# Kernel tuning notes

Hardware: AMD Instinct MI355X
Metric: run time of the kernel (lower is better)

The kernel has to match this reference:

```python
import jax, jax.numpy as jnp
import numpy as np

N_NODES = 100000
N_EDGES = 1600000  # undirected edges (incidence rows)
F_IN, HID, N_CLS = 500, 256, 40
K_ITERS = 5
LAMBDA1 = 3.0
LAMBDA2 = 3.0


def setup_inputs() -> dict:
    key = jax.random.key(0)
    k1, k2, k3, k4, k5 = jax.random.split(key, 5)
    x = jax.random.normal(k1, (N_NODES, F_IN), dtype=jnp.float32)
    W1 = jax.random.normal(k2, (F_IN, HID), dtype=jnp.float32) * 0.05
    W2 = jax.random.normal(k3, (HID, N_CLS), dtype=jnp.float32) * 0.05
    src = jax.random.randint(k4, (N_EDGES,), 0, N_NODES, dtype=jnp.int32)
    off = jax.random.randint(k5, (N_EDGES,), 1, N_NODES, dtype=jnp.int32)
    dst = (src + off) % N_NODES  # avoid self-edges
    return {"x": x, "W1": W1, "W2": W2, "src": src, "dst": dst}


def reference(x, W1, W2, src, dst):
    N = x.shape[0]
    # --- MLP (eval mode: dropout is identity) ---
    h = jnp.maximum(x @ W1, 0.0)
    h = h @ W2  # [N, C]

    # --- gcn_norm: A_hat = D^{-1/2}(A + I)D^{-1/2}, deg from A + I ---
    rows = jnp.concatenate([src, dst])  # symmetric adjacency
    cols = jnp.concatenate([dst, src])
    deg = jax.ops.segment_sum(jnp.ones(rows.shape[0], x.dtype), rows,
                              num_segments=N) + 1.0
    dis = deg ** -0.5  # deg_inv_sqrt, [N]
    edge_val = dis[rows] * dis[cols]
    self_val = dis * dis

    def spmm(v):  # A_hat @ v
        return (jax.ops.segment_sum(edge_val[:, None] * v[cols], rows,
                                    num_segments=N) + self_val[:, None] * v)

    # normalized incidence: inc[e, src]=dis[src], inc[e, dst]=-dis[dst]
    def inc_t(z):  # inc.T @ z -> [N, C]
        return dis[:, None] * (jax.ops.segment_sum(z, src, num_segments=N)
                               - jax.ops.segment_sum(z, dst, num_segments=N))

    def inc(v):  # inc @ v -> [E, C]
        vs = dis[:, None] * v
        return vs[src] - vs[dst]

    gamma = 1.0 / (1.0 + LAMBDA2)
    beta = 1.0 / (2.0 * gamma)

    hh = h
    xc = h
    z = jnp.zeros((src.shape[0], h.shape[1]), h.dtype)
    for _ in range(K_ITERS):
        y = gamma * hh + (1.0 - gamma) * spmm(xc)
        x_bar = y - gamma * inc_t(z)
        z_bar = z + beta * inc(x_bar)
        # L21 proximal projection: clamp row norms at lambda1
        rn = jnp.linalg.norm(z_bar, axis=1)
        scale = jnp.where(rn > 0,
                          jnp.minimum(rn, LAMBDA1) / jnp.where(rn > 0, rn, 1.0),
                          0.0)
        z = scale[:, None] * z_bar
        xc = y - gamma * inc_t(z)
        # F.dropout with training=False is identity
    return jax.nn.log_softmax(xc, axis=1)
```

## Files before the change

kernel.cpp:

```cpp
#include <hip/hip_runtime.h>
#include <hip/hip_fp16.h>
#include <math.h>

#define NN 100000
#define NE 1600000
#define FIN 500
#define HID 256
#define NC 40
#define NC2 20
#define KIT 5
#define L1P 3.0f
#define GAM 0.25f
#define BET 2.0f
#define OMG 0.75f
#define PADH2 32

__global__ void k_hist(const int* __restrict__ s, const int* __restrict__ d, int* cs, int* cd) {
    int e = blockIdx.x * 256 + threadIdx.x;
    if (e < NE) { atomicAdd(&cs[s[e]], 1); atomicAdd(&cd[d[e]], 1); }
}

__global__ void k_scan1(const int* __restrict__ cnt, int* rp, int* bs) {
    __shared__ int sm[1024];
    int i = blockIdx.x * 1024 + threadIdx.x;
    int v = (i < NN) ? cnt[i] : 0;
    sm[threadIdx.x] = v;
    __syncthreads();
    for (int off = 1; off < 1024; off <<= 1) {
        int t = (threadIdx.x >= off) ? sm[threadIdx.x - off] : 0;
        __syncthreads();
        sm[threadIdx.x] += t;
        __syncthreads();
    }
    if (i < NN) rp[i] = sm[threadIdx.x] - v;
    if (threadIdx.x == 1023) bs[blockIdx.x] = sm[1023];
}

__global__ void k_scan2(int* bs, int nb) {
    if (threadIdx.x == 0 && blockIdx.x == 0) {
        int run = 0;
        for (int j = 0; j < nb; j++) { int t = bs[j]; bs[j] = run; run += t; }
    }
}

__global__ void k_scan3(int* rp, const int* __restrict__ bs, int total) {
    int i = blockIdx.x * 1024 + threadIdx.x;
    if (i < NN) rp[i] += bs[blockIdx.x];
    if (i == 0) rp[NN] = total;
}

__global__ void k_dis(const int* __restrict__ cs, const int* __restrict__ cd, float* __restrict__ dis) {
    int n = blockIdx.x * 256 + threadIdx.x;
    if (n < NN) dis[n] = rsqrtf((float)(cs[n] + cd[n]) + 1.0f);
}

__global__ void k_fillp(const int* __restrict__ s, const int* __restrict__ d,
                        const int* __restrict__ rps, const int* __restrict__ rpd,
                        int* curs, int* curd,
                        int* sa, int* sb, int* pd, int* da) {
    int e = blockIdx.x * 256 + threadIdx.x;
    if (e < NE) {
        int a = s[e], b = d[e];
        int i = rps[a] + atomicAdd(&curs[a], 1);
        int j = rpd[b] + atomicAdd(&curd[b], 1);
        sa[i] = a; sb[i] = b; pd[i] = j; da[j] = a;
    }
}

__global__ __launch_bounds__(256) void k_gemm1(const float* __restrict__ X,
                                               const float* __restrict__ W1,
                                               float* __restrict__ H1) {
    __shared__ float As[8][128];
    __shared__ float Bs[8][128];
    const int t = threadIdx.x;
    const int rblk = blockIdx.x * 128;
    const int cblk = blockIdx.y * 128;
    const int tx = t & 15, ty = t >> 4;
    const int lar = t >> 1, lak = (t & 1) * 4;
    const int lbk = t >> 5, lbc = (t & 31) * 4;
    float acc[8][8];
    #pragma unroll
    for (int i = 0; i < 8; i++)
        #pragma unroll
        for (int j = 0; j < 8; j++) acc[i][j] = 0.f;

    for (int k0 = 0; k0 < FIN; k0 += 8) {
        float4 av = make_float4(0.f, 0.f, 0.f, 0.f);
        int row = rblk + lar;
        if (row < NN) {
            if (k0 + lak + 4 <= FIN) {
                av = *(const float4*)(X + (size_t)row * FIN + k0 + lak);
            } else {
                float tv[4] = {0.f, 0.f, 0.f, 0.f};
                #pragma unroll
                for (int j = 0; j < 4; j++)
                    if (k0 + lak + j < FIN) tv[j] = X[(size_t)row * FIN + k0 + lak + j];
                av = make_float4(tv[0], tv[1], tv[2], tv[3]);
            }
        }
        As[lak + 0][lar] = av.x; As[lak + 1][lar] = av.y;
        As[lak + 2][lar] = av.z; As[lak + 3][lar] = av.w;

        float4 bv = make_float4(0.f, 0.f, 0.f, 0.f);
        if (k0 + lbk < FIN) bv = *(const float4*)(W1 + (size_t)(k0 + lbk) * HID + cblk + lbc);
        *(float4*)&Bs[lbk][lbc] = bv;
        __syncthreads();

        #pragma unroll
        for (int kk = 0; kk < 8; kk++) {
            float aF[8], bF[8];
            *(float4*)&aF[0] = *(const float4*)&As[kk][ty * 4];
            *(float4*)&aF[4] = *(const float4*)&As[kk][64 + ty * 4];
            *(float4*)&bF[0] = *(const float4*)&Bs[kk][tx * 4];
            *(float4*)&bF[4] = *(const float4*)&Bs[kk][64 + tx * 4];
            #pragma unroll
            for (int i = 0; i < 8; i++)
                #pragma unroll
                for (int j = 0; j < 8; j++)
                    acc[i][j] = fmaf(aF[i], bF[j], acc[i][j]);
        }
        __syncthreads();
    }

    #pragma unroll
    for (int i = 0; i < 8; i++) {
        int row = rblk + ((i < 4) ? (ty * 4 + i) : (64 + ty * 4 + (i - 4)));
        if (row < NN) {
            float4 v0, v1;
            v0.x = fmaxf(acc[i][0], 0.f); v0.y = fmaxf(acc[i][1], 0.f);
            v0.z = fmaxf(acc[i][2], 0.f); v0.w = fmaxf(acc[i][3], 0.f);
            v1.x = fmaxf(acc[i][4], 0.f); v1.y = fmaxf(acc[i][5], 0.f);
            v1.z = fmaxf(acc[i][6], 0.f); v1.w = fmaxf(acc[i][7], 0.f);
            *(float4*)(H1 + (size_t)row * HID + cblk + tx * 4) = v0;
            *(float4*)(H1 + (size_t)row * HID + cblk + 64 + tx * 4) = v1;
        }
    }
}

__global__ __launch_bounds__(256) void k_gemm2(const float* __restrict__ H1,
                                               const float* __restrict__ W2,
                                               const float* __restrict__ dis,
                                               float* __restrict__ hh, __half2* __restrict__ xg2) {
    __shared__ float w2s[HID * NC];
    for (int i = threadIdx.x; i < HID * NC; i += 256) w2s[i] = W2[i];
    __syncthreads();
    int wave = threadIdx.x >> 6, lane = threadIdx.x & 63;
    int n = blockIdx.x * 4 + wave;
    if (n >= NN) return;
    if (lane < NC) {
        const float* hr = H1 + (size_t)n * HID;
        float acc = 0.f;
        #pragma unroll 4
        for (int k = 0; k < HID; k += 4) {
            float4 h4 = *(const float4*)(hr + k);
            acc = fmaf(h4.x, w2s[(k + 0) * NC + lane], acc);
            acc = fmaf(h4.y, w2s[(k + 1) * NC + lane], acc);
            acc = fmaf(h4.z, w2s[(k + 2) * NC + lane], acc);
            acc = fmaf(h4.w, w2s[(k + 3) * NC + lane], acc);
        }
        hh[(size_t)n * NC + lane] = acc;
        ((__half*)xg2)[(size_t)n * (2 * PADH2) + lane] = __float2half_rn(dis[n] * acc);
    }
}

__global__ __launch_bounds__(256) void k_ynew(const int* __restrict__ rps, const int* __restrict__ rpd,
                                              const int* __restrict__ sb, const int* __restrict__ da,
                                              const float* __restrict__ dis, const float2* __restrict__ hh2,
                                              const float2* __restrict__ S2, const __half2* __restrict__ xg2,
                                              float2* __restrict__ y2, __half2* __restrict__ xbs2) {
    int wave = threadIdx.x >> 6, lane = threadIdx.x & 63;
    int g = lane >> 5, sl = lane & 31;
    int n = blockIdx.x * 4 + wave;
    if (n >= NN) return;
    bool act = sl < NC2;
    float accx = 0.f, accy = 0.f;

    int p = rps[n] + g, e0 = rps[n + 1];
    for (; p + 2 < e0; p += 4) {
        int c0 = sb[p], c1 = sb[p + 2];
        if (act) {
            float2 v0 = __half22float2(xg2[(size_t)c0 * PADH2 + sl]);
            float2 v1 = __half22float2(xg2[(size_t)c1 * PADH2 + sl]);
            accx += v0.x + v1.x; accy += v0.y + v1.y;
        }
    }
    if (p < e0) {
        int c = sb[p];
        if (act) {
            float2 v = __half22float2(xg2[(size_t)c * PADH2 + sl]);
            accx += v.x; accy += v.y;
        }
    }
    p = rpd[n] + g; e0 = rpd[n + 1];
    for (; p + 2 < e0; p += 4) {
        int c0 = da[p], c1 = da[p + 2];
        if (act) {
            float2 v0 = __half22float2(xg2[(size_t)c0 * PADH2 + sl]);
            float2 v1 = __half22float2(xg2[(size_t)c1 * PADH2 + sl]);
            accx += v0.x + v1.x; accy += v0.y + v1.y;
        }
    }
    if (p < e0) {
        int c = da[p];
        if (act) {
            float2 v = __half22float2(xg2[(size_t)c * PADH2 + sl]);
            accx += v.x; accy += v.y;
        }
    }
    accx += __shfl_xor(accx, 32);
    accy += __shfl_xor(accy, 32);
    if (act && g == 0) {
        float2 self = __half22float2(xg2[(size_t)n * PADH2 + sl]);
        accx += self.x; accy += self.y;
        size_t b2 = (size_t)n * NC2 + sl;
        float dn = dis[n];
        float2 h = hh2[b2], Sv = S2[b2];
        float yx = GAM * h.x + OMG * dn * accx;
        float yy = GAM * h.y + OMG * dn * accy;
        y2[b2] = make_float2(yx, yy);
        xbs2[(size_t)n * PADH2 + sl] = __float22half2_rn(
            make_float2(dn * (yx - GAM * dn * Sv.x), dn * (yy - GAM * dn * Sv.y)));
    }
}

__global__ __launch_bounds__(256) void k_zup(const int* __restrict__ sa, const int* __restrict__ sb,
                                             const int* __restrict__ pd, const __half2* __restrict__ xbs2,
                                             __half2* __restrict__ zs2, __half2* __restrict__ zd2, int use_z) {
    int wid = (blockIdx.x * 256 + threadIdx.x) >> 6;
    int lane = threadIdx.x & 63;
    int g = lane >> 5, sl = lane & 31;
    long i = (long)wid * 2 + g;
    if (i >= NE) return;
    int a = sa[i], b = sb[i], j = pd[i];
    float zx = 0.f, zy = 0.f;
    bool act = sl < NC2;
    if (act) {
        float2 ia = __half22float2(xbs2[(size_t)a * PADH2 + sl]);
        float2 ib = __half22float2(xbs2[(size_t)b * PADH2 + sl]);
        float2 zv = make_float2(0.f, 0.f);
        if (use_z) zv = __half22float2(zs2[(size_t)i * NC2 + sl]);
        zx = zv.x + BET * (ia.x - ib.x);
        zy = zv.y + BET * (ia.y - ib.y);
    }
    float n2 = zx * zx + zy * zy;
    #pragma unroll
    for (int off = 1; off < 32; off <<= 1) n2 += __shfl_xor(n2, off, 32);
    float rn = sqrtf(n2);
    float sc = (rn > L1P) ? (L1P / rn) : 1.0f;
    if (act) {
        __half2 hv = __float22half2_rn(make_float2(zx * sc, zy * sc));
        zs2[(size_t)i * NC2 + sl] = hv;
        zd2[(size_t)j * NC2 + sl] = hv;
    }
}

__global__ __launch_bounds__(256) void k_scx(const int* __restrict__ rps, const int* __restrict__ rpd,
                                             const __half2* __restrict__ zs2, const __half2* __restrict__ zd2,
                                             const float2* __restrict__ y2, const float* __restrict__ dis,
                                             float2* __restrict__ S2, float2* __restrict__ xc2,
                                             __half2* __restrict__ xg2) {
    int wave = threadIdx.x >> 6, lane = threadIdx.x & 63;
    int g = lane >> 5, sl = lane & 31;
    int n = blockIdx.x * 4 + wave;
    if (n >= NN) return;
    bool act = sl < NC2;
    float accx = 0.f, accy = 0.f;

    int p = rps[n] + g, e0 = rps[n + 1];
    for (; p + 2 < e0; p += 4) {
        if (act) {
            float2 v0 = __half22float2(zs2[(size_t)p * NC2 + sl]);
            float2 v1 = __half22float2(zs2[(size_t)(p + 2) * NC2 + sl]);
            accx += v0.x + v1.x; accy += v0.y + v1.y;
        }
    }
    if (p < e0 && act) {
        float2 v = __half22float2(zs2[(size_t)p * NC2 + sl]);
        accx += v.x; accy += v.y;
    }
    p = rpd[n] + g; e0 = rpd[n + 1];
    for (; p + 2 < e0; p += 4) {
        if (act) {
            float2 v0 = __half22float2(zd2[(size_t)p * NC2 + sl]);
            float2 v1 = __half22float2(zd2[(size_t)(p + 2) * NC2 + sl]);
            accx -= v0.x + v1.x; accy -= v0.y + v1.y;
        }
    }
    if (p < e0 && act) {
        float2 v = __half22float2(zd2[(size_t)p * NC2 + sl]);
        accx -= v.x; accy -= v.y;
    }
    accx += __shfl_xor(accx, 32);
    accy += __shfl_xor(accy, 32);
    if (act && g == 0) {
        size_t b2 = (size_t)n * NC2 + sl;
        float dn = dis[n];
        float2 yv = y2[b2];
        float vx = yv.x - GAM * dn * accx;
        float vy = yv.y - GAM * dn * accy;
        S2[b2] = make_float2(accx, accy);
        xc2[b2] = make_float2(vx, vy);
        xg2[(size_t)n * PADH2 + sl] = __float22half2_rn(make_float2(dn * vx, dn * vy));
    }
}

__global__ __launch_bounds__(256) void k_lsm(const float* __restrict__ xc, float* __restrict__ out) {
    int wave = threadIdx.x >> 6, lane = threadIdx.x & 63;
    int n = blockIdx.x * 4 + wave;
    if (n >= NN) return;
    float v = (lane < NC) ? xc[(size_t)n * NC + lane] : -INFINITY;
    float m = v;
    #pragma unroll
    for (int off = 1; off < 64; off <<= 1) m = fmaxf(m, __shfl_xor(m, off));
    float ex = (lane < NC) ? expf(v - m) : 0.f;
    float ssum = ex;
    #pragma unroll
    for (int off = 1; off < 64; off <<= 1) ssum += __shfl_xor(ssum, off);
    if (lane < NC) out[(size_t)n * NC + lane] = v - m - logf(ssum);
}

extern "C" void kernel_launch(void* const* d_in, const int* in_sizes, int n_in,
                              void* d_out, int out_size, void* d_ws, size_t ws_size,
                              hipStream_t stream) {
    const float* x  = (const float*)d_in[0];
    const float* W1 = (const float*)d_in[1];
    const float* W2 = (const float*)d_in[2];
    const int* src  = (const int*)d_in[3];
    const int* dst  = (const int*)d_in[4];
    float* out = (float*)d_out;

    char* w = (char*)d_ws;
    auto alloc = [&](size_t bytes) { char* p = w; w += (bytes + 255) & ~(size_t)255; return p; };
    float* dis   = (float*)alloc((size_t)NN * 4);
    int*   cs    = (int*)  alloc((size_t)NN * 4);
    int*   cd    = (int*)  alloc((size_t)NN * 4);
    int*   curs  = (int*)  alloc((size_t)NN * 4);
    int*   curd  = (int*)  alloc((size_t)NN * 4);
    int*   rps   = (int*)  alloc((size_t)(NN + 1) * 4);
    int*   rpd   = (int*)  alloc((size_t)(NN + 1) * 4);
    int*   bs    = (int*)  alloc(1024 * 4);
    int*   sa    = (int*)  alloc((size_t)NE * 4);
    int*   sb    = (int*)  alloc((size_t)NE * 4);
    int*   pd    = (int*)  alloc((size_t)NE * 4);
    int*   da    = (int*)  alloc((size_t)NE * 4);
    float* hh    = (float*)alloc((size_t)NN * NC * 4);
    float* xc    = (float*)alloc((size_t)NN * NC * 4);
    float* yb    = (float*)alloc((size_t)NN * NC * 4);
    float* S     = (float*)alloc((size_t)NN * NC * 4);
    __half2* xg  = (__half2*)alloc((size_t)NN * PADH2 * 4);
    __half2* xbs = (__half2*)alloc((size_t)NN * PADH2 * 4);
    __half2* zs  = (__half2*)alloc((size_t)NE * NC2 * 4);
    __half2* zd  = (__half2*)alloc((size_t)NE * NC2 * 4);
    float* h1    = (float*)zs;

    hipMemsetAsync(cs, 0, (size_t)NN * 4, stream);
    hipMemsetAsync(cd, 0, (size_t)NN * 4, stream);
    hipMemsetAsync(curs, 0, (size_t)NN * 4, stream);
    hipMemsetAsync(curd, 0, (size_t)NN * 4, stream);
    k_hist<<<(NE + 255) / 256, 256, 0, stream>>>(src, dst, cs, cd);
    int nb = (NN + 1023) / 1024;
    k_scan1<<<nb, 1024, 0, stream>>>(cs, rps, bs);
    k_scan2<<<1, 64, 0, stream>>>(bs, nb);
    k_scan3<<<nb, 1024, 0, stream>>>(rps, bs, NE);
    k_scan1<<<nb, 1024, 0, stream>>>(cd, rpd, bs);
    k_scan2<<<1, 64, 0, stream>>>(bs, nb);
    k_scan3<<<nb, 1024, 0, stream>>>(rpd, bs, NE);
    k_dis<<<(NN + 255) / 256, 256, 0, stream>>>(cs, cd, dis);
    k_fillp<<<(NE + 255) / 256, 256, 0, stream>>>(src, dst, rps, rpd, curs, curd, sa, sb, pd, da);

    k_gemm1<<<dim3((NN + 127) / 128, HID / 128), 256, 0, stream>>>(x, W1, h1);
    k_gemm2<<<(NN + 3) / 4, 256, 0, stream>>>(h1, W2, dis, hh, xg);

    hipMemsetAsync(S, 0, (size_t)NN * NC * 4, stream);
    int zblocks = (int)(((size_t)NE / 2 + 3) / 4);
    for (int t = 0; t < KIT; t++) {
        k_ynew<<<(NN + 3) / 4, 256, 0, stream>>>(rps, rpd, sb, da, dis, (const float2*)hh,
                                                 (const float2*)S, xg, (float2*)yb, xbs);
        k_zup<<<zblocks, 256, 0, stream>>>(sa, sb, pd, xbs, zs, zd, t > 0 ? 1 : 0);
        k_scx<<<(NN + 3) / 4, 256, 0, stream>>>(rps, rpd, zs, zd, (const float2*)yb, dis,
                                                (float2*)S, (float2*)xc, xg);
    }
    k_lsm<<<(NN + 3) / 4, 256, 0, stream>>>(xc, out);
}
```

Baseline: 3.675 ms.

## Run first MLP GEMM on bf16 MFMA with hi/lo split emulation

Result: no change. 3.612 ms (-1.7%).

```diff
diff --git a/kernel.cpp b/kernel.cpp
--- a/kernel.cpp
+++ b/kernel.cpp
@@ -5,6 +5,7 @@
 #define NN 100000
 #define NE 1600000
 #define FIN 500
+#define FINP 512
 #define HID 256
 #define NC 40
 #define NC2 20
@@ -14,6 +15,19 @@
 #define BET 2.0f
 #define OMG 0.75f
 #define PADH2 32
+
+typedef short bf16x8 __attribute__((ext_vector_type(8)));
+typedef unsigned short us8 __attribute__((ext_vector_type(8)));
+typedef float f32x4 __attribute__((ext_vector_type(4)));
+
+__device__ inline void split_bf16(float x, unsigned short& hi, unsigned short& lo) {
+    unsigned u = __float_as_uint(x);
+    hi = (unsigned short)(u >> 16);
+    float r = x - __uint_as_float(u & 0xFFFF0000u);
+    unsigned ur = __float_as_uint(r);
+    ur += 0x8000u + ((ur >> 16) & 1u);
+    lo = (unsigned short)(ur >> 16);
+}
 
 __global__ void k_hist(const int* __restrict__ s, const int* __restrict__ d, int* cs, int* cd) {
     int e = blockIdx.x * 256 + threadIdx.x;
@@ -67,72 +81,82 @@
     }
 }
 
-__global__ __launch_bounds__(256) void k_gemm1(const float* __restrict__ X,
-                                               const float* __restrict__ W1,
-                                               float* __restrict__ H1) {
-    __shared__ float As[8][128];
-    __shared__ float Bs[8][128];
+__global__ void k_splitW(const float* __restrict__ W1, unsigned short* __restrict__ Wh,
+                         unsigned short* __restrict__ Wl) {
+    int idx = blockIdx.x * 256 + threadIdx.x;
+    if (idx >= HID * FINP) return;
+    int kk = idx >> 8;
+    int n  = idx & (HID - 1);
+    float v = (kk < FIN) ? W1[(size_t)kk * HID + n] : 0.f;
+    unsigned short h, l;
+    split_bf16(v, h, l);
+    Wh[(size_t)n * FINP + kk] = h;
+    Wl[(size_t)n * FINP + kk] = l;
+}
+
+__global__ __launch_bounds__(256) void k_gemm1m(const float* __restrict__ X,
+                                                const unsigned short* __restrict__ W1h,
+                                                const unsigned short* __restrict__ W1l,
+                                                float* __restrict__ H1) {
+    __shared__ unsigned short Ah[32][40], Al[32][40];
+    __shared__ unsigned short Bh[256][40], Bl[256][40];
     const int t = threadIdx.x;
-    const int rblk = blockIdx.x * 128;
-    const int cblk = blockIdx.y * 128;
-    const int tx = t & 15, ty = t >> 4;
-    const int lar = t >> 1, lak = (t & 1) * 4;
-    const int lbk = t >> 5, lbc = (t & 31) * 4;
-    float acc[8][8];
+    const int rblk = blockIdx.x * 32;
+    const int lane = t & 63, wv = t >> 6;
+    const int mw = (wv >> 1) * 16;
+    const int nw = (wv & 1) * 128;
+    const int l15 = lane & 15, kg = lane >> 4;
+
+    f32x4 acc[8];
     #pragma unroll
-    for (int i = 0; i < 8; i++)
+    for (int i = 0; i < 8; i++) acc[i] = (f32x4){0.f, 0.f, 0.f, 0.f};
+
+    const int ar = t >> 3;
+    const int ak = (t & 7) * 4;
+    const int grow = rblk + ar;
+
+    for (int ks = 0; ks < 16; ks++) {
+        const int k0 = ks * 32;
+        __syncthreads();
+        {
+            float4 v = make_float4(0.f, 0.f, 0.f, 0.f);
+            if (grow < NN && k0 + ak < FIN)
+                v = *(const float4*)(X + (size_t)grow * FIN + k0 + ak);
+            ushort4 h4, l4;
+            split_bf16(v.x, h4.x, l4.x); split_bf16(v.y, h4.y, l4.y);
+            split_bf16(v.z, h4.z, l4.z); split_bf16(v.w, h4.w, l4.w);
+            *(ushort4*)&Ah[ar][ak] = h4;
+            *(ushort4*)&Al[ar][ak] = l4;
+        }
+        {
+            const size_t wb = (size_t)t * FINP + k0;
+            #pragma unroll
+            for (int q = 0; q < 4; q++) {
+                *(us8*)&Bh[t][q * 8] = *(const us8*)&W1h[wb + q * 8];
+                *(us8*)&Bl[t][q * 8] = *(const us8*)&W1l[wb + q * 8];
+            }
+        }
+        __syncthreads();
+        bf16x8 a_h = *(const bf16x8*)&Ah[mw + l15][kg * 8];
+        bf16x8 a_l = *(const bf16x8*)&Al[mw + l15][kg * 8];
         #pragma unroll
-        for (int j = 0; j < 8; j++) acc[i][j] = 0.f;
-
-    for (int k0 = 0; k0 < FIN; k0 += 8) {
-        float4 av = make_float4(0.f, 0.f, 0.f, 0.f);
-        int row = rblk + lar;
-        if (row < NN) {
-            if (k0 + lak + 4 <= FIN) {
-                av = *(const float4*)(X + (size_t)row * FIN + k0 + lak);
-            } else {
-                float tv[4] = {0.f, 0.f, 0.f, 0.f};
-                #pragma unroll
-                for (int j = 0; j < 4; j++)
-                    if (k0 + lak + j < FIN) tv[j] = X[(size_t)row * FIN + k0 + lak + j];
-                av = make_float4(tv[0], tv[1], tv[2], tv[3]);
-            }
-        }
-        As[lak + 0][lar] = av.x; As[lak + 1][lar] = av.y;
-        As[lak + 2][lar] = av.z; As[lak + 3][lar] = av.w;
-
-        float4 bv = make_float4(0.f, 0.f, 0.f, 0.f);
-        if (k0 + lbk < FIN) bv = *(const float4*)(W1 + (size_t)(k0 + lbk) * HID + cblk + lbc);
-        *(float4*)&Bs[lbk][lbc] = bv;
-        __syncthreads();
-
-        #pragma unroll
-        for (int kk = 0; kk < 8; kk++) {
-            float aF[8], bF[8];
-            *(float4*)&aF[0] = *(const float4*)&As[kk][ty * 4];
-            *(float4*)&aF[4] = *(const float4*)&As[kk][64 + ty * 4];
-            *(float4*)&bF[0] = *(const float4*)&Bs[kk][tx * 4];
-            *(float4*)&bF[4] = *(const float4*)&Bs[kk][64 + tx * 4];
+        for (int nt = 0; nt < 8; nt++) {
+            int n = nw + nt * 16 + l15;
+            bf16x8 b_h = *(const bf16x8*)&Bh[n][kg * 8];
+            bf16x8 b_l = *(const bf16x8*)&Bl[n][kg * 8];
+            acc[nt] = __builtin_amdgcn_mfma_f32_16x16x32_bf16(a_h, b_h, acc[nt], 0, 0, 0);
+            acc[nt] = __builtin_amdgcn_mfma_f32_16x16x32_bf16(a_h, b_l, acc[nt], 0, 0, 0);
+            acc[nt] = __builtin_amdgcn_mfma_f32_16x16x32_bf16(a_l, b_h, acc[nt], 0, 0, 0);
+        }
+    }
+    const int orow = rblk + mw + kg * 4;
+    #pragma unroll
+    for (int reg = 0; reg < 4; reg++) {
+        int gr = orow + reg;
+        if (gr < NN) {
             #pragma unroll
-            for (int i = 0; i < 8; i++)
-                #pragma unroll
-                for (int j = 0; j < 8; j++)
-                    acc[i][j] = fmaf(aF[i], bF[j], acc[i][j]);
-        }
-        __syncthreads();
-    }
-
-    #pragma unroll
-    for (int i = 0; i < 8; i++) {
-        int row = rblk + ((i < 4) ? (ty * 4 + i) : (64 + ty * 4 + (i - 4)));
-        if (row < NN) {
-            float4 v0, v1;
-            v0.x = fmaxf(acc[i][0], 0.f); v0.y = fmaxf(acc[i][1], 0.f);
-            v0.z = fmaxf(acc[i][2], 0.f); v0.w = fmaxf(acc[i][3], 0.f);
-            v1.x = fmaxf(acc[i][4], 0.f); v1.y = fmaxf(acc[i][5], 0.f);
-            v1.z = fmaxf(acc[i][6], 0.f); v1.w = fmaxf(acc[i][7], 0.f);
-            *(float4*)(H1 + (size_t)row * HID + cblk + tx * 4) = v0;
-            *(float4*)(H1 + (size_t)row * HID + cblk + 64 + tx * 4) = v1;
+            for (int nt = 0; nt < 8; nt++)
+                H1[(size_t)gr * HID + nw + nt * 16 + l15] = fmaxf(acc[nt][reg], 0.f);
         }
     }
 }
@@ -343,6 +367,8 @@
     int*   sb    = (int*)  alloc((size_t)NE * 4);
     int*   pd    = (int*)  alloc((size_t)NE * 4);
     int*   da    = (int*)  alloc((size_t)NE * 4);
+    unsigned short* W1h = (unsigned short*)alloc((size_t)HID * FINP * 2);
+    unsigned short* W1l = (unsigned short*)alloc((size_t)HID * FINP * 2);
     float* hh    = (float*)alloc((size_t)NN * NC * 4);
     float* xc    = (float*)alloc((size_t)NN * NC * 4);
     float* yb    = (float*)alloc((size_t)NN * NC * 4);
@@ -368,7 +394,8 @@
     k_dis<<<(NN + 255) / 256, 256, 0, stream>>>(cs, cd, dis);
     k_fillp<<<(NE + 255) / 256, 256, 0, stream>>>(src, dst, rps, rpd, curs, curd, sa, sb, pd, da);
 
-    k_gemm1<<<dim3((NN + 127) / 128, HID / 128), 256, 0, stream>>>(x, W1, h1);
+    k_splitW<<<(HID * FINP + 255) / 256, 256, 0, stream>>>(W1, W1h, W1l);
+    k_gemm1m<<<(NN + 31) / 32, 256, 0, stream>>>(x, W1h, W1l, h1);
     k_gemm2<<<(NN + 3) / 4, 256, 0, stream>>>(h1, W2, dis, hh, xg);
 
     hipMemsetAsync(S, 0, (size_t)NN * NC * 4, stream);
```
